# Kernel tuning notes

Hardware: AMD Instinct MI355X
Metric: run time of the kernel (lower is better)

## Reference

```python
import jax, jax.numpy as jnp
import numpy as np

N = 100000
E = 1600000
D_IN = 128
D_HID = 128
D_OUT = 16


def setup_inputs() -> dict:
    key = jax.random.key(0)
    ks = jax.random.split(key, 10)
    x = jax.random.normal(ks[0], (N, D_IN), dtype=jnp.float32)
    edge_index = jax.random.randint(ks[1], (2, E), 0, N, dtype=jnp.int32)
    s = 1.0 / np.sqrt(D_IN)
    sh = 1.0 / np.sqrt(D_HID)
    W1l = jax.random.uniform(ks[2], (D_HID, D_IN), jnp.float32, -s, s)
    b1l = jax.random.uniform(ks[3], (D_HID,), jnp.float32, -s, s)
    W1r = jax.random.uniform(ks[4], (D_HID, D_IN), jnp.float32, -s, s)
    W2l = jax.random.uniform(ks[5], (D_HID, D_HID), jnp.float32, -sh, sh)
    b2l = jax.random.uniform(ks[6], (D_HID,), jnp.float32, -sh, sh)
    W2r = jax.random.uniform(ks[7], (D_HID, D_HID), jnp.float32, -sh, sh)
    Wc = jax.random.uniform(ks[8], (D_OUT, D_HID), jnp.float32, -sh, sh)
    bc = jax.random.uniform(ks[9], (D_OUT,), jnp.float32, -sh, sh)
    return {"x": x, "edge_index": edge_index, "W1l": W1l, "b1l": b1l, "W1r": W1r,
            "W2l": W2l, "b2l": b2l, "W2r": W2r, "Wc": Wc, "bc": bc}


def _sage_conv(x, src, dst, Wl, bl, Wr):
    # PyG SAGEConv (mean aggr): out_i = Wl @ mean_{j in N(i)} x_j + bl + Wr @ x_i
    n = x.shape[0]
    msg = x[src]                                             # [E, d] gather
    summed = jax.ops.segment_sum(msg, dst, num_segments=n)   # [N, d] scatter-add
    cnt = jax.ops.segment_sum(jnp.ones((src.shape[0],), x.dtype), dst, num_segments=n)
    agg = summed / jnp.maximum(cnt, 1.0)[:, None]            # mean; isolated nodes -> 0
    return agg @ Wl.T + bl + x @ Wr.T


def reference(x, edge_index, W1l, b1l, W1r, W2l, b2l, W2r, Wc, bc):
    src, dst = edge_index[0], edge_index[1]
    h = jax.nn.relu(_sage_conv(x, src, dst, W1l, b1l, W1r))
    # dropout p=0.5 is identity at inference (training=False)
    z = _sage_conv(h, src, dst, W2l, b2l, W2r)
    return z @ Wc.T + bc
```

## Files before the change

### kernel.cpp

```cpp
#include <hip/hip_runtime.h>

#define BSHIFT 8
#define MAXB   512
#define BPAD   16
#define BCAP   6912
#define CHUNK  8192

typedef __bf16 bf16x8 __attribute__((ext_vector_type(8)));
typedef float  f32x4  __attribute__((ext_vector_type(4)));
typedef float  f32x2  __attribute__((ext_vector_type(2)));

__device__ __forceinline__ unsigned short f2b(float f) {
  unsigned u = __float_as_uint(f);
  return (unsigned short)((u + 0x7fffu + ((u >> 16) & 1u)) >> 16);
}
__device__ __forceinline__ float b2f_lo(unsigned u) {
  return __uint_as_float(u << 16);
}
__device__ __forceinline__ float b2f_hi(unsigned u) {
  return __uint_as_float(u & 0xffff0000u);
}

__global__ __launch_bounds__(1024) void k_bin(
    const int* __restrict__ ei, int E, int* __restrict__ bcnt,
    unsigned* __restrict__ edg,
    const float* __restrict__ W1l, const float* __restrict__ W1r,
    unsigned short* __restrict__ Wb,
    const float* __restrict__ Wc, const float* __restrict__ bc,
    const float* __restrict__ W2l, const float* __restrict__ W2r,
    const float* __restrict__ b2, unsigned short* __restrict__ Mb,
    float* __restrict__ bias2,
    unsigned short* __restrict__ xb, unsigned* __restrict__ xq,
    unsigned short* __restrict__ Pnb, int ZR, int nbin) {
  __shared__ int lh[MAXB], lbase[MAXB], lcur[MAXB];
  __shared__ int ldst[CHUNK];
  const int b = blockIdx.x;
  const int t = threadIdx.x;
  if (b < nbin) {
    for (int i = t; i < MAXB; i += 1024) { lh[i] = 0; lcur[i] = 0; }
    __syncthreads();
    const int e0 = b * CHUNK;
    const int n = min(E - e0, CHUNK);
    const int* __restrict__ src = ei;
    const int* __restrict__ dst = ei + E;
    for (int j = t; j < n; j += 1024) {
      int d = dst[e0 + j];
      ldst[j] = d;
      atomicAdd(&lh[((unsigned)d) >> BSHIFT], 1);
    }
    __syncthreads();
    for (int i = t; i < MAXB; i += 1024)
      if (lh[i]) lbase[i] = atomicAdd(&bcnt[i * BPAD], lh[i]);
    __syncthreads();
    for (int j = t; j < n; j += 1024) {
      int d = ldst[j];
      unsigned s = (unsigned)src[e0 + j];
      int bk = ((unsigned)d) >> BSHIFT;
      int p = lbase[bk] + atomicAdd(&lcur[bk], 1);
      if (p < BCAP) edg[(size_t)bk * BCAP + p] = ((unsigned)(d & 255) << 17) | s;
    }
  } else if (t < 256) {
    int bb = b - nbin;
    if (bb < 128) {
      int idx = bb * 256 + t;
      int col = idx >> 8, k = idx & 255;
      float v = (k < 128) ? W1l[col * 128 + k] : W1r[col * 128 + (k - 128)];
      Wb[col * 256 + k] = f2b(v);
    } else if (bb < 144) {
      int mb = bb - 128;
      int mat = mb >> 3;
      const float* W2 = mat ? W2r : W2l;
      int o = (mb & 7) * 2 + (t >> 7);
      int k = t & 127;
      float s = 0.f;
      for (int j = 0; j < 128; ++j) s = fmaf(Wc[o * 128 + j], W2[j * 128 + k], s);
      Mb[(size_t)(mat * 16 + o) * 128 + k] = f2b(s);
      if (mb == 0 && t < 16) {
        float sb = bc[t];
        for (int j = 0; j < 128; ++j) sb = fmaf(Wc[t * 128 + j], b2[j], sb);
        bias2[t] = sb;
      }
    } else {
      if (t < 64) ((unsigned*)(xb + (size_t)ZR * 128))[t] = 0;
      if (t < 32) xq[(size_t)ZR * 32 + t] = 0;
      if (t < 8)  ((unsigned*)(Pnb + (size_t)ZR * 16))[t] = 0;
    }
  }
}

__global__ __launch_bounds__(1024) void k_buildcast(
    const unsigned* __restrict__ edg, const int* __restrict__ bcnt,
    int* __restrict__ eidx, int* __restrict__ rowcnt, int N, int ZR,
    int nbuck, const float* __restrict__ x, unsigned short* __restrict__ xb,
    unsigned* __restrict__ xq, int ngroups) {
  __shared__ int lsrc[BCAP];
  __shared__ int lcnt[256], lstart[256], lcur[256];
  __shared__ int wsum[4];
  const int b = blockIdx.x;
  const int t = threadIdx.x;
  if (b >= nbuck) {
    int g = (b - nbuck) * 1024 + t;
    if (g < ngroups) {
      float4 v = ((const float4*)x)[g];
      ushort4 o;
      o.x = f2b(v.x); o.y = f2b(v.y); o.z = f2b(v.z); o.w = f2b(v.w);
      ((ushort4*)xb)[g] = o;
      int q8 = __builtin_amdgcn_cvt_pk_fp8_f32(v.x, v.y, 0, false);
      q8 = __builtin_amdgcn_cvt_pk_fp8_f32(v.z, v.w, q8, true);
      xq[g] = (unsigned)q8;
    }
    return;
  }
  const int node0 = b << BSHIFT;
  const int nb = min(256, N - node0);
  const int ecount = min(bcnt[b * BPAD], BCAP);
  const unsigned* __restrict__ ed = edg + (size_t)b * BCAP;
  if (t < 256) lcnt[t] = 0;
  __syncthreads();
  for (int j = t; j < ecount; j += 1024)
    atomicAdd(&lcnt[ed[j] >> 17], 1);
  __syncthreads();
  int incl = 0, pad = 0;
  if (t < 256) {
    int c = lcnt[t];
    pad = (c + 15) & ~15;
    incl = pad;
    int lane = t & 63;
#pragma unroll
    for (int off = 1; off < 64; off <<= 1) {
      int v = __shfl_up(incl, off, 64);
      if (lane >= off) incl += v;
    }
    if (lane == 63) wsum[t >> 6] = incl;
  }
  __syncthreads();
  if (t < 256) {
    int wv = t >> 6;
    int woff = 0;
    for (int i = 0; i < wv; ++i) woff += wsum[i];
    int excl = woff + incl - pad;
    lstart[t] = excl; lcur[t] = excl;
  }
  __syncthreads();
  for (int j = t; j < ecount; j += 1024) {
    unsigned e = ed[j];
    int p = atomicAdd(&lcur[e >> 17], 1);
    lsrc[p] = (int)(e & 0x1FFFFu);
  }
  if (t < 256) {
    int c = lcnt[t];
    int s0 = lstart[t] + c;
    int s1 = lstart[t] + ((c + 15) & ~15);
    for (int j = s0; j < s1; ++j) lsrc[j] = ZR;
  }
  __syncthreads();
  const int ebase = b * BCAP;
  int tot = wsum[0] + wsum[1] + wsum[2] + wsum[3];
  int ecountp = min(tot, BCAP);
  for (int j = 4 * t; j < ecountp; j += 4096) {
    int4 v = *(const int4*)&lsrc[j];
    *(int4*)&eidx[ebase + j] = v;
  }
  if (t < nb) {
    rowcnt[2 * (node0 + t)]     = ebase + lstart[t];
    rowcnt[2 * (node0 + t) + 1] = lcnt[t];
  }
}

__global__ __launch_bounds__(256) void k_agg1(
    const int* __restrict__ eidx, const int* __restrict__ rowcnt,
    const unsigned* __restrict__ xq, unsigned short* __restrict__ aggb, int N) {
  int wv = (blockIdx.x * 256 + threadIdx.x) >> 6;
  int lane = threadIdx.x & 63;
  const int sub = lane >> 4;
  const int li  = lane & 15;
  int n = wv * 4 + sub;
  const bool act = (n < N);
  int deg = 0;
  const int* el = eidx;
  if (act) {
    int2 rc = *(const int2*)(rowcnt + 2 * (size_t)n);
    deg = rc.y;
    el = eidx + rc.x;
  }
  f32x2 acc[4];
#pragma unroll
  for (int j = 0; j < 4; ++j) acc[j] = (f32x2){0.f, 0.f};

  for (int e = 0; e < deg; e += 4) {
    int4 q = *(const int4*)(el + e);
    uint2 v0 = *(const uint2*)(xq + (size_t)q.x * 32 + li * 2);
    uint2 v1 = *(const uint2*)(xq + (size_t)q.y * 32 + li * 2);
    uint2 v2 = *(const uint2*)(xq + (size_t)q.z * 32 + li * 2);
    uint2 v3 = *(const uint2*)(xq + (size_t)q.w * 32 + li * 2);
#define ADD8(v)                                                      \
    acc[0] += __builtin_amdgcn_cvt_pk_f32_fp8(v.x, false);           \
    acc[1] += __builtin_amdgcn_cvt_pk_f32_fp8(v.x, true);            \
    acc[2] += __builtin_amdgcn_cvt_pk_f32_fp8(v.y, false);           \
    acc[3] += __builtin_amdgcn_cvt_pk_f32_fp8(v.y, true);
    ADD8(v0) ADD8(v1) ADD8(v2) ADD8(v3)
#undef ADD8
  }
  if (act) {
    float sc = 1.0f / (float)max(deg, 1);
    uint4 o4;
    o4.x = (unsigned)f2b(acc[0].x * sc) | ((unsigned)f2b(acc[0].y * sc) << 16);
    o4.y = (unsigned)f2b(acc[1].x * sc) | ((unsigned)f2b(acc[1].y * sc) << 16);
    o4.z = (unsigned)f2b(acc[2].x * sc) | ((unsigned)f2b(acc[2].y * sc) << 16);
    o4.w = (unsigned)f2b(acc[3].x * sc) | ((unsigned)f2b(acc[3].y * sc) << 16);
    *(uint4*)(aggb + (size_t)n * 128 + li * 8) = o4;
  }
}

__global__ __launch_bounds__(256) void k_gemm1_mfma(
    const unsigned short* __restrict__ aggb, const unsigned short* __restrict__ xb,
    const unsigned short* __restrict__ Wb, const float* __restrict__ b1,
    const unsigned short* __restrict__ Mb,
    unsigned short* __restrict__ Pnb, float* __restrict__ Ps, int N) {
  __shared__ union {
    struct { unsigned short A[128 * 40]; unsigned short W[128 * 40]; } s;
    unsigned short H[128 * 136];
  } sm;
  const int t = threadIdx.x;
  const int w = t >> 6;
  const int lane = t & 63;
  const int q = lane >> 4;
  const int l16 = lane & 15;
  const int row0 = blockIdx.x * 128;

  f32x4 acc[2][8];
#pragma unroll
  for (int rt = 0; rt < 2; ++rt)
#pragma unroll
    for (int ct = 0; ct < 8; ++ct) acc[rt][ct] = (f32x4){0.f, 0.f, 0.f, 0.f};

  for (int kc = 0; kc < 8; ++kc) {
    const unsigned short* Asrc = (kc < 4) ? aggb : xb;
    const int koff = (kc & 3) * 32;
#pragma unroll
    for (int i = 0; i < 2; ++i) {
      int idx = t + i * 256;
      int row = idx >> 2, c4 = idx & 3;
      int gr = row0 + row; if (gr >= N) gr = N - 1;
      uint4 v = *(const uint4*)(Asrc + (size_t)gr * 128 + koff + c4 * 8);
      *(uint4*)(sm.s.A + row * 40 + c4 * 8) = v;
    }
#pragma unroll
    for (int i = 0; i < 2; ++i) {
      int idx = t + i * 256;
      int col = idx >> 2, c4 = idx & 3;
      uint4 v = *(const uint4*)(Wb + col * 256 + kc * 32 + c4 * 8);
      *(uint4*)(sm.s.W + col * 40 + c4 * 8) = v;
    }
    __syncthreads();
    bf16x8 afr[2];
#pragma unroll
    for (int rt = 0; rt < 2; ++rt)
      afr[rt] = *(const bf16x8*)(sm.s.A + (w * 32 + rt * 16 + l16) * 40 + q * 8);
    bf16x8 bfr[8];
#pragma unroll
    for (int ct = 0; ct < 8; ++ct)
      bfr[ct] = *(const bf16x8*)(sm.s.W + (ct * 16 + l16) * 40 + q * 8);
#pragma unroll
    for (int rt = 0; rt < 2; ++rt)
#pragma unroll
      for (int ct = 0; ct < 8; ++ct)
        acc[rt][ct] = __builtin_amdgcn_mfma_f32_16x16x32_bf16(
            afr[rt], bfr[ct], acc[rt][ct], 0, 0, 0);
    __syncthreads();
  }

  float bv[8];
#pragma unroll
  for (int ct = 0; ct < 8; ++ct) bv[ct] = b1[ct * 16 + l16];
#pragma unroll
  for (int rt = 0; rt < 2; ++rt) {
    int rl = w * 32 + rt * 16 + q * 4;
#pragma unroll
    for (int reg = 0; reg < 4; ++reg) {
#pragma unroll
      for (int ct = 0; ct < 8; ++ct) {
        float v = acc[rt][ct][reg] + bv[ct];
        sm.H[(rl + reg) * 136 + ct * 16 + l16] = f2b(v > 0.f ? v : 0.f);
      }
    }
  }
  __syncthreads();

  f32x4 acc2[2][2];
#pragma unroll
  for (int rt = 0; rt < 2; ++rt)
#pragma unroll
    for (int ct = 0; ct < 2; ++ct) acc2[rt][ct] = (f32x4){0.f, 0.f, 0.f, 0.f};
#pragma unroll
  for (int ks = 0; ks < 4; ++ks) {
    bf16x8 a2[2], b2v[2];
#pragma unroll
    for (int rt = 0; rt < 2; ++rt)
      a2[rt] = *(const bf16x8*)(sm.H + (w * 32 + rt * 16 + l16) * 136 + ks * 32 + q * 8);
#pragma unroll
    for (int ct = 0; ct < 2; ++ct)
      b2v[ct] = *(const bf16x8*)(Mb + (size_t)(ct * 16 + l16) * 128 + ks * 32 + q * 8);
#pragma unroll
    for (int rt = 0; rt < 2; ++rt)
#pragma unroll
      for (int ct = 0; ct < 2; ++ct)
        acc2[rt][ct] = __builtin_amdgcn_mfma_f32_16x16x32_bf16(
            a2[rt], b2v[ct], acc2[rt][ct], 0, 0, 0);
  }
#pragma unroll
  for (int rt = 0; rt < 2; ++rt) {
    int rbase = row0 + w * 32 + rt * 16 + q * 4;
#pragma unroll
    for (int reg = 0; reg < 4; ++reg) {
      int r = rbase + reg;
      Pnb[(size_t)r * 16 + l16] = f2b(acc2[rt][0][reg]);
      Ps[(size_t)r * 16 + l16] = acc2[rt][1][reg];
    }
  }
}

__global__ __launch_bounds__(256) void k_agg2_out(
    const int* __restrict__ eidx, const int* __restrict__ rowcnt,
    const unsigned short* __restrict__ Pnb, const float* __restrict__ Ps,
    const float* __restrict__ bias2, float* __restrict__ out, int N) {
  int i = (blockIdx.x * 256 + threadIdx.x) >> 6;
  int lane = threadIdx.x & 63;
  if (i >= N) return;
  const int sub = lane >> 2;
  const int li = lane & 3;
  int2 rc = *(const int2*)(rowcnt + 2 * (size_t)i);
  int deg = rc.y;
  const int* el = eidx + rc.x;
  f32x2 a0 = (f32x2){0.f, 0.f}, a1 = (f32x2){0.f, 0.f};
  for (int e = 0; e < deg; e += 16) {
    if (e + sub < deg) {
      int idx = el[e + sub];
      uint2 v = *(const uint2*)(Pnb + (size_t)idx * 16 + li * 4);
      a0 += (f32x2){b2f_lo(v.x), b2f_hi(v.x)};
      a1 += (f32x2){b2f_lo(v.y), b2f_hi(v.y)};
    }
  }
#pragma unroll
  for (int m = 4; m <= 32; m <<= 1) {
    a0.x += __shfl_xor(a0.x, m, 64);
    a0.y += __shfl_xor(a0.y, m, 64);
    a1.x += __shfl_xor(a1.x, m, 64);
    a1.y += __shfl_xor(a1.y, m, 64);
  }
  if (sub == 0) {
    float sc = 1.0f / (float)max(deg, 1);
    float4 self = *(const float4*)(Ps + (size_t)i * 16 + li * 4);
    float4 b = *(const float4*)(bias2 + li * 4);
    float4 o;
    o.x = a0.x * sc + self.x + b.x;
    o.y = a0.y * sc + self.y + b.y;
    o.z = a1.x * sc + self.z + b.z;
    o.w = a1.y * sc + self.w + b.w;
    *(float4*)(out + (size_t)i * 16 + li * 4) = o;
  }
}

extern "C" void kernel_launch(void* const* d_in, const int* in_sizes, int n_in,
                              void* d_out, int out_size, void* d_ws, size_t ws_size,
                              hipStream_t stream) {
  const float* x   = (const float*)d_in[0];
  const int*   ei  = (const int*)d_in[1];
  const float* W1l = (const float*)d_in[2];
  const float* b1l = (const float*)d_in[3];
  const float* W1r = (const float*)d_in[4];
  const float* W2l = (const float*)d_in[5];
  const float* b2l = (const float*)d_in[6];
  const float* W2r = (const float*)d_in[7];
  const float* Wc  = (const float*)d_in[8];
  const float* bc  = (const float*)d_in[9];
  float* out = (float*)d_out;

  const int N      = in_sizes[0] / 128;
  const int E      = in_sizes[1] / 2;
  const int Np     = ((N + 127) / 128) * 128;
  const int NBUCK  = (N + 255) >> BSHIFT;
  const int ZR     = Np;
  const int NBIN   = (E + CHUNK - 1) / CHUNK;
  const int NCAST  = (N * 32 + 1023) / 1024;

  char* ws = (char*)d_ws;
  size_t off = 0;
  auto alloc = [&](size_t bytes) {
    void* p = ws + off;
    off = (off + bytes + 255) & ~(size_t)255;
    return p;
  };
  int*            rowcnt   = (int*)           alloc((size_t)N * 8);
  int*            bcnt     = (int*)           alloc((size_t)MAXB * BPAD * 4);
  unsigned*       edg      = (unsigned*)      alloc((size_t)NBUCK * BCAP * 4);
  int*            eidx     = (int*)           alloc((size_t)NBUCK * BCAP * 4);
  unsigned short* xb       = (unsigned short*)alloc((size_t)(Np + 1) * 128 * 2);
  unsigned*       xq       = (unsigned*)      alloc((size_t)(Np + 1) * 32 * 4);
  unsigned short* aggb     = (unsigned short*)alloc((size_t)Np * 128 * 2);
  unsigned short* Wb       = (unsigned short*)alloc((size_t)128 * 256 * 2);
  unsigned short* Mb       = (unsigned short*)alloc((size_t)32 * 128 * 2);
  unsigned short* Pnb      = (unsigned short*)alloc((size_t)(Np + 1) * 16 * 2);
  float*          Ps       = (float*)         alloc((size_t)Np * 16 * 4);
  float*          bias2    = (float*)         alloc(16 * 4);
  (void)ws_size; (void)n_in; (void)out_size;

  hipMemsetAsync(bcnt, 0, (size_t)MAXB * BPAD * 4, stream);
  k_bin<<<NBIN + 145, 1024, 0, stream>>>(
      ei, E, bcnt, edg,
      W1l, W1r, Wb, Wc, bc, W2l, W2r, b2l, Mb, bias2, xb, xq, Pnb, ZR, NBIN);
  k_buildcast<<<NBUCK + NCAST, 1024, 0, stream>>>(
      edg, bcnt, eidx, rowcnt, N, ZR, NBUCK, x, xb, xq, N * 32);
  k_agg1<<<(N + 15) / 16, 256, 0, stream>>>(eidx, rowcnt, xq, aggb, N);
  k_gemm1_mfma<<<Np / 128, 256, 0, stream>>>(aggb, xb, Wb, b1l, Mb, Pnb, Ps, N);
  k_agg2_out<<<(N + 3) / 4, 256, 0, stream>>>(eidx, rowcnt, Pnb, Ps, bias2, out, N);
}
```

Measured before the change: 229.9 us.

## Map one node per 4-lane group in second aggregation, unroll neighbor loads by four

The final aggregation kernel now assigns each node to a 4-lane group, so a wave handles 16 nodes instead of one. This removes the cross-lane shuffle reduction and the idle lanes on low-degree nodes. Each group reads neighbor indices four at a time with an int4 load and issues four row gathers per iteration. This relies on the edge lists being padded to a multiple of four, with padding pointing at a zero row, and on their start offsets being 16-byte aligned. Lanes within a wave now loop for different degrees, which causes divergence.

```diff
diff --git a/kernel.cpp b/kernel.cpp
--- a/kernel.cpp
+++ b/kernel.cpp
@@ -324,40 +324,42 @@
     const int* __restrict__ eidx, const int* __restrict__ rowcnt,
     const unsigned short* __restrict__ Pnb, const float* __restrict__ Ps,
     const float* __restrict__ bias2, float* __restrict__ out, int N) {
-  int i = (blockIdx.x * 256 + threadIdx.x) >> 6;
+  int wv = (blockIdx.x * 256 + threadIdx.x) >> 6;
   int lane = threadIdx.x & 63;
-  if (i >= N) return;
   const int sub = lane >> 2;
-  const int li = lane & 3;
-  int2 rc = *(const int2*)(rowcnt + 2 * (size_t)i);
-  int deg = rc.y;
-  const int* el = eidx + rc.x;
+  const int li  = lane & 3;
+  int n = wv * 16 + sub;
+  const bool act = (n < N);
+  int deg = 0;
+  const int* el = eidx;
+  if (act) {
+    int2 rc = *(const int2*)(rowcnt + 2 * (size_t)n);
+    deg = rc.y;
+    el = eidx + rc.x;
+  }
   f32x2 a0 = (f32x2){0.f, 0.f}, a1 = (f32x2){0.f, 0.f};
-  for (int e = 0; e < deg; e += 16) {
-    if (e + sub < deg) {
-      int idx = el[e + sub];
-      uint2 v = *(const uint2*)(Pnb + (size_t)idx * 16 + li * 4);
-      a0 += (f32x2){b2f_lo(v.x), b2f_hi(v.x)};
-      a1 += (f32x2){b2f_lo(v.y), b2f_hi(v.y)};
-    }
-  }
-#pragma unroll
-  for (int m = 4; m <= 32; m <<= 1) {
-    a0.x += __shfl_xor(a0.x, m, 64);
-    a0.y += __shfl_xor(a0.y, m, 64);
-    a1.x += __shfl_xor(a1.x, m, 64);
-    a1.y += __shfl_xor(a1.y, m, 64);
-  }
-  if (sub == 0) {
+  for (int e = 0; e < deg; e += 4) {
+    int4 q = *(const int4*)(el + e);
+    uint2 v0 = *(const uint2*)(Pnb + (size_t)q.x * 16 + li * 4);
+    uint2 v1 = *(const uint2*)(Pnb + (size_t)q.y * 16 + li * 4);
+    uint2 v2 = *(const uint2*)(Pnb + (size_t)q.z * 16 + li * 4);
+    uint2 v3 = *(const uint2*)(Pnb + (size_t)q.w * 16 + li * 4);
+#define ACC2(v)                                   \
+    a0 += (f32x2){b2f_lo(v.x), b2f_hi(v.x)};      \
+    a1 += (f32x2){b2f_lo(v.y), b2f_hi(v.y)};
+    ACC2(v0) ACC2(v1) ACC2(v2) ACC2(v3)
+#undef ACC2
+  }
+  if (act) {
     float sc = 1.0f / (float)max(deg, 1);
-    float4 self = *(const float4*)(Ps + (size_t)i * 16 + li * 4);
+    float4 self = *(const float4*)(Ps + (size_t)n * 16 + li * 4);
     float4 b = *(const float4*)(bias2 + li * 4);
     float4 o;
     o.x = a0.x * sc + self.x + b.x;
     o.y = a0.y * sc + self.y + b.y;
     o.z = a1.x * sc + self.z + b.z;
     o.w = a1.y * sc + self.w + b.w;
-    *(float4*)(out + (size_t)i * 16 + li * 4) = o;
+    *(float4*)(out + (size_t)n * 16 + li * 4) = o;
   }
 }
 
@@ -413,5 +415,5 @@
       edg, bcnt, eidx, rowcnt, N, ZR, NBUCK, x, xb, xq, N * 32);
   k_agg1<<<(N + 15) / 16, 256, 0, stream>>>(eidx, rowcnt, xq, aggb, N);
   k_gemm1_mfma<<<Np / 128, 256, 0, stream>>>(aggb, xb, Wb, b1l, Mb, Pnb, Ps, N);
-  k_agg2_out<<<(N + 3) / 4, 256, 0, stream>>>(eidx, rowcnt, Pnb, Ps, bias2, out, N);
-}
+  k_agg2_out<<<(N + 63) / 64, 256, 0, stream>>>(eidx, rowcnt, Pnb, Ps, bias2, out, N);
+}
```

Result: faster. 216.9 us (-5.7%).
